# Kernel optimization log

Measured on AMD Instinct MI355X. Metric: run time of the kernel, lower is better.

The kernel has to match this reference:

```python
import jax, jax.numpy as jnp
import numpy as np

MARGIN = 0.3
EPS = 1e-12


def setup_inputs() -> dict:
    key = jax.random.key(0)
    k1, k2, k3, k4 = jax.random.split(key, 4)
    B, N, D = 4, 6400, 32
    pred_masks = jax.random.normal(k1, (B, N, D), dtype=jnp.float32)
    pos_rand = jax.random.uniform(k2, (B, N), dtype=jnp.float32)
    target_gt_idx = jax.random.randint(k3, (B, N), 0, 20, dtype=jnp.int64)
    fg_mask = jax.random.randint(k4, (B, N), 0, 2) > 0
    return {
        "pred_masks": pred_masks,
        "pos_rand": pos_rand,
        "target_gt_idx": target_gt_idx,
        "fg_mask": fg_mask,
    }


def reference(pred_masks, pos_rand, target_gt_idx, fg_mask):
    B, N, D = pred_masks.shape
    # L2-normalize coefficients (F.normalize, eps=1e-12)
    norm = jnp.sqrt(jnp.sum(pred_masks * pred_masks, axis=-1, keepdims=True))
    coeffs = pred_masks / jnp.maximum(norm, EPS)  # [B,N,D]

    valid_pair = fg_mask[:, :, None] & fg_mask[:, None, :]  # [B,N,N]
    same_inst = target_gt_idx[:, :, None] == target_gt_idx[:, None, :]
    eye = jnp.eye(N, dtype=bool)
    S = valid_pair & same_inst & ~eye          # positives (same instance, not self)
    Dm = valid_pair & ~same_inst               # negatives (different instance)

    # Cosine similarities (vectors are unit norm)
    sims = jnp.einsum('bnd,bmd->bnm', coeffs, coeffs)  # [B,N,N]

    # Hardest negative per anchor: argmax similarity among negatives
    neg_idx = jnp.argmax(jnp.where(Dm, sims, -jnp.inf), axis=-1)  # [B,N]
    neg_vec = jnp.take_along_axis(coeffs, neg_idx[..., None], axis=1)  # [B,N,D]

    # Random positive: pick the k-th positive in anchor order, k = floor(u*num_pos)
    num_pos = jnp.sum(S, axis=-1)  # [B,N]
    pos_choice = jnp.floor(pos_rand * num_pos.astype(pos_rand.dtype)).astype(jnp.int32)
    pos_choice = jnp.clip(pos_choice, 0, jnp.maximum(num_pos - 1, 0).astype(jnp.int32))
    cum = jnp.cumsum(S.astype(jnp.int32), axis=-1)  # rank of each positive
    sel = S & (cum == (pos_choice + 1)[..., None])  # one-hot over chosen positive
    pos_idx = jnp.argmax(sel, axis=-1)  # [B,N]
    pos_vec = jnp.take_along_axis(coeffs, pos_idx[..., None], axis=1)  # [B,N,D]

    pos_d = jnp.sqrt(jnp.sum((coeffs - pos_vec) ** 2, axis=-1) + EPS)
    neg_d = jnp.sqrt(jnp.sum((coeffs - neg_vec) ** 2, axis=-1) + EPS)

    valid = fg_mask & (num_pos >= 1) & jnp.any(Dm, axis=-1)  # anchor forms a triplet
    per_anchor = jnp.maximum(pos_d - neg_d + MARGIN, 0.0)
    n_trip = jnp.sum(valid)
    total = jnp.sum(per_anchor * valid.astype(per_anchor.dtype))
    return jnp.where(n_trip > 0, total / jnp.maximum(n_trip, 1).astype(total.dtype), 0.0)
```

## Files before the change

kernel.cpp:

```cpp
#include <hip/hip_runtime.h>
#include <math.h>

#define B_ 4
#define N_ 6400
#define D_ 32
#define TJ 256
#define NCHJ 25
#define TI 128
#define CHUNK 256
#define NCC 25

typedef __attribute__((ext_vector_type(4))) float f32x4;
typedef __attribute__((ext_vector_type(8))) short bf16x8;

static constexpr float MARGIN_ = 0.3f;

__device__ __forceinline__ unsigned fmap(float f) {
    unsigned u = __float_as_uint(f);
    return (u & 0x80000000u) ? ~u : (u | 0x80000000u);
}
__device__ __forceinline__ float funmap(unsigned u) {
    return (u & 0x80000000u) ? __uint_as_float(u ^ 0x80000000u)
                             : __uint_as_float(~u);
}
#define NEG_INF_MAPPED 0x007FFFFFu

__device__ __forceinline__ unsigned short f2bf(float f) {
    unsigned u = __float_as_uint(f);
    unsigned r = u + 0x7fffu + ((u >> 16) & 1u);
    return (unsigned short)(r >> 16);
}
__device__ __forceinline__ float bf2f(unsigned short h) {
    return __uint_as_float(((unsigned)h) << 16);
}
__device__ __forceinline__ void bf2x(unsigned u, float& e0, float& e1) {
    e0 = __uint_as_float(u << 16);
    e1 = __uint_as_float(u & 0xffff0000u);
}

__global__ __launch_bounds__(256) void k_prep(const float* __restrict__ pred,
                                              const int* __restrict__ gt,
                                              const int* __restrict__ fg,
                                              unsigned short* __restrict__ hi_g,
                                              unsigned short* __restrict__ lo_g,
                                              int* __restrict__ clist,
                                              int* __restrict__ cg,
                                              int* __restrict__ Marr,
                                              unsigned* __restrict__ bestArr) {
    int c = blockIdx.x, b = blockIdx.y;
    int t = threadIdx.x;
    int lane = t & 63, w = t >> 6;
    int idx = c * CHUNK + t;

    bestArr[b * N_ + idx] = NEG_INF_MAPPED;

    bool flag = fg[b * N_ + idx] != 0;
    unsigned long long m = __ballot(flag);
    int lp = __popcll(m & ((1ull << lane) - 1ull));
    __shared__ int wsh[4];
    __shared__ int s_off, s_M;
    if (lane == 0) wsh[w] = __popcll(m);

    if (w == 0) {
        int pre = 0, tot = 0;
        #pragma unroll
        for (int cc = 0; cc < NCC; ++cc) {
            const int4 v = ((const int4*)(fg + (size_t)b * N_ + cc * CHUNK))[lane];
            int cnt = (v.x != 0) + (v.y != 0) + (v.z != 0) + (v.w != 0);
            #pragma unroll
            for (int o = 1; o < 64; o <<= 1) cnt += __shfl_xor(cnt, o);
            pre += (cc < c) ? cnt : 0;
            tot += cnt;
        }
        if (lane == 0) { s_off = pre; s_M = tot; }
    }
    __syncthreads();
    if (c == 0 && t == 0) Marr[b] = s_M;
    if (!flag) return;

    int woff = 0;
    #pragma unroll
    for (int k = 0; k < 4; ++k) if (k < w) woff += wsh[k];
    int rank = s_off + woff + lp;
    clist[b * N_ + rank] = idx;
    cg[b * N_ + rank] = gt[b * N_ + idx];

    const float4* s4 = (const float4*)(pred + ((size_t)b * N_ + idx) * D_);
    float f[32];
    float ssq = 0.0f;
    #pragma unroll
    for (int k = 0; k < 8; ++k) {
        float4 q = s4[k];
        f[k * 4] = q.x; f[k * 4 + 1] = q.y; f[k * 4 + 2] = q.z; f[k * 4 + 3] = q.w;
        ssq += q.x * q.x + q.y * q.y + q.z * q.z + q.w * q.w;
    }
    float inv = 1.0f / fmaxf(sqrtf(ssq), 1e-12f);
    unsigned hw[16], lw[16];
    #pragma unroll
    for (int k = 0; k < 16; ++k) {
        float x0 = f[2 * k] * inv, x1 = f[2 * k + 1] * inv;
        unsigned short h0 = f2bf(x0), h1 = f2bf(x1);
        unsigned short l0 = f2bf(x0 - bf2f(h0)), l1 = f2bf(x1 - bf2f(h1));
        hw[k] = (unsigned)h0 | ((unsigned)h1 << 16);
        lw[k] = (unsigned)l0 | ((unsigned)l1 << 16);
    }
    uint4* dh = (uint4*)(hi_g + ((size_t)b * N_ + rank) * 32);
    uint4* dl = (uint4*)(lo_g + ((size_t)b * N_ + rank) * 32);
    #pragma unroll
    for (int k = 0; k < 4; ++k) {
        dh[k] = make_uint4(hw[4 * k], hw[4 * k + 1], hw[4 * k + 2], hw[4 * k + 3]);
        dl[k] = make_uint4(lw[4 * k], lw[4 * k + 1], lw[4 * k + 2], lw[4 * k + 3]);
    }
}

__global__ __launch_bounds__(256) void k_pass(const unsigned short* __restrict__ hi_g,
                                              const unsigned short* __restrict__ lo_g,
                                              const int* __restrict__ cg,
                                              const int* __restrict__ Marr,
                                              unsigned short* __restrict__ p_cnt,
                                              unsigned* __restrict__ bestArr) {
    int b = blockIdx.z;
    int M = Marr[b];
    int i0 = blockIdx.x * TI;
    int j0 = blockIdx.y * TJ;
    if (i0 >= M || j0 >= M) return;

    __shared__ __align__(16) unsigned short sc_hi[TJ * 40];
    __shared__ __align__(16) unsigned short sc_lo[TJ * 40];
    __shared__ int sg[TJ];
    int t = threadIdx.x;

    {
        int j = j0 + t;
        sg[t] = (j < M) ? cg[b * N_ + j] : -1;
    }
    {
        int seg = t & 3, r0 = t >> 2;
        #pragma unroll
        for (int p = 0; p < 4; ++p) {
            int row = p * 64 + r0;
            int j = j0 + row;
            uint4 vh = make_uint4(0u, 0u, 0u, 0u), vl = make_uint4(0u, 0u, 0u, 0u);
            if (j < M) {
                vh = *(const uint4*)(hi_g + ((size_t)b * N_ + j) * 32 + seg * 8);
                vl = *(const uint4*)(lo_g + ((size_t)b * N_ + j) * 32 + seg * 8);
            }
            *(uint4*)(sc_hi + row * 40 + seg * 8) = vh;
            *(uint4*)(sc_lo + row * 40 + seg * 8) = vl;
        }
    }
    __syncthreads();

    int lane = t & 63, w = t >> 6;
    int r = lane & 15, quad = lane >> 4;
    int ib = i0 + w * 32;

    bf16x8 a_hi[2], a_lo[2];
    int gt_i[2][4];
    #pragma unroll
    for (int it = 0; it < 2; ++it) {
        int i = ib + it * 16 + r;
        bf16x8 zh = {0, 0, 0, 0, 0, 0, 0, 0};
        a_hi[it] = zh; a_lo[it] = zh;
        if (i < M) {
            a_hi[it] = *(const bf16x8*)(hi_g + ((size_t)b * N_ + i) * 32 + quad * 8);
            a_lo[it] = *(const bf16x8*)(lo_g + ((size_t)b * N_ + i) * 32 + quad * 8);
        }
        #pragma unroll
        for (int r4 = 0; r4 < 4; ++r4) {
            int ia = ib + it * 16 + quad * 4 + r4;
            gt_i[it][r4] = (ia < M) ? cg[b * N_ + ia] : -2;
        }
    }

    float best[2][4];
    int cnt[2][4];
    #pragma unroll
    for (int it = 0; it < 2; ++it)
        #pragma unroll
        for (int r4 = 0; r4 < 4; ++r4) { best[it][r4] = -INFINITY; cnt[it][r4] = 0; }

    int jrows = min(TJ, M - j0);
    int ntile = (jrows + 15) >> 4;
    for (int jt = 0; jt < ntile; ++jt) {
        int gtj = sg[jt * 16 + r];
        bf16x8 bh = *(const bf16x8*)(sc_hi + (jt * 16 + r) * 40 + quad * 8);
        bf16x8 bl = *(const bf16x8*)(sc_lo + (jt * 16 + r) * 40 + quad * 8);
        bool jv = (gtj >= 0);
        #pragma unroll
        for (int it = 0; it < 2; ++it) {
            f32x4 acc = {0.f, 0.f, 0.f, 0.f};
            acc = __builtin_amdgcn_mfma_f32_16x16x32_bf16(a_hi[it], bh, acc, 0, 0, 0);
            acc = __builtin_amdgcn_mfma_f32_16x16x32_bf16(a_hi[it], bl, acc, 0, 0, 0);
            acc = __builtin_amdgcn_mfma_f32_16x16x32_bf16(a_lo[it], bh, acc, 0, 0, 0);
            #pragma unroll
            for (int r4 = 0; r4 < 4; ++r4) {
                float s = acc[r4];
                bool same = (gtj == gt_i[it][r4]);
                float sm = (same || !jv) ? -INFINITY : s;
                best[it][r4] = fmaxf(best[it][r4], sm);
                cnt[it][r4] += same ? 1 : 0;
            }
        }
    }

    #pragma unroll
    for (int it = 0; it < 2; ++it) {
        #pragma unroll
        for (int r4 = 0; r4 < 4; ++r4) {
            float bb = best[it][r4];
            int cc = cnt[it][r4];
            #pragma unroll
            for (int mk = 1; mk < 16; mk <<= 1) {
                bb = fmaxf(bb, __shfl_xor(bb, mk));
                cc += __shfl_xor(cc, mk);
            }
            if (r == 0) {
                int ia = ib + it * 16 + quad * 4 + r4;
                if (ia < M) {
                    p_cnt[((size_t)b * N_ + ia) * NCHJ + blockIdx.y] = (unsigned short)cc;
                    if (bb > -INFINITY) atomicMax(&bestArr[b * N_ + ia], fmap(bb));
                }
            }
        }
    }
}

__global__ __launch_bounds__(256) void k_combine(const unsigned short* __restrict__ hi_g,
                                                 const unsigned short* __restrict__ lo_g,
                                                 const int* __restrict__ cg,
                                                 const int* __restrict__ clist,
                                                 const int* __restrict__ Marr,
                                                 const float* __restrict__ pos_rand,
                                                 const unsigned short* __restrict__ p_cnt,
                                                 const unsigned* __restrict__ bestArr,
                                                 float* __restrict__ cArr,
                                                 int* __restrict__ vArr) {
    int b = blockIdx.y;
    int M = Marr[b];
    int t = threadIdx.x;
    int w = t >> 6, lane = t & 63;
    int i = blockIdx.x * 4 + w;

    if (i >= M) return;

    float contrib = 0.0f;
    int vflag = 0;

    int nchj = (M + TJ - 1) / TJ;
    int ich = i / TJ;
    const unsigned short* pc = p_cnt + ((size_t)b * N_ + i) * NCHJ;
    int c_s = 0;
    if (lane < nchj) c_s = (int)pc[lane] - (lane == ich ? 1 : 0);
    int P = c_s;
    #pragma unroll
    for (int off = 1; off < 64; off <<= 1) {
        int n = __shfl_up(P, off);
        if (lane >= off) P += n;
    }
    int num_pos = __shfl(P, 63);
    unsigned bu = bestArr[b * N_ + i];
    if (num_pos >= 1 && bu != NEG_INF_MAPPED) {
        float best = funmap(bu);
        int orig = clist[b * N_ + i];
        float u = pos_rand[b * N_ + orig];
        int pcx = (int)floorf(u * (float)num_pos);
        int hi2 = num_pos - 1;
        pcx = pcx < 0 ? 0 : (pcx > hi2 ? hi2 : pcx);
        int target = pcx + 1;
        unsigned long long selm = __ballot(P >= target);
        int sstar = __ffsll((unsigned long long)selm) - 1;
        int c0 = (sstar > 0) ? __shfl(P, sstar - 1) : 0;
        int need = target - c0;
        int jstart = sstar * TJ;
        int jend = min(jstart + TJ, M);
        int ga = cg[b * N_ + i];
        int posj = -1;
        #pragma unroll
        for (int k = 0; k < 4; ++k) {
            if (posj >= 0) continue;
            int j = jstart + k * 64 + lane;
            bool flag = (j < jend) && (cg[b * N_ + j] == ga) && (j != i);
            unsigned long long mk = __ballot(flag);
            int tot = __popcll(mk);
            if (need <= tot) {
                int pfx = __popcll(mk & ((1ull << lane) - 1ull));
                unsigned long long sel = __ballot(flag && (pfx == need - 1));
                posj = jstart + k * 64 + (__ffsll((unsigned long long)sel) - 1);
            } else {
                need -= tot;
            }
        }
        float part = 0.0f;
        if (lane < 16) {
            unsigned xh = ((const unsigned*)(hi_g + ((size_t)b * N_ + i) * 32))[lane];
            unsigned xl = ((const unsigned*)(lo_g + ((size_t)b * N_ + i) * 32))[lane];
            unsigned yh = ((const unsigned*)(hi_g + ((size_t)b * N_ + posj) * 32))[lane];
            unsigned yl = ((const unsigned*)(lo_g + ((size_t)b * N_ + posj) * 32))[lane];
            float a0, a1, b0, b1, c0f, c1f, d0, d1;
            bf2x(xh, a0, a1); bf2x(xl, b0, b1);
            bf2x(yh, c0f, c1f); bf2x(yl, d0, d1);
            part = fmaf(a0 + b0, c0f + d0, (a1 + b1) * (c1f + d1));
        }
        #pragma unroll
        for (int mk2 = 1; mk2 < 16; mk2 <<= 1) part += __shfl_xor(part, mk2);
        float dot = part;
        float pos_d = sqrtf(fmaxf(2.f - 2.f * dot, 0.f) + 1e-12f);
        float neg_d = sqrtf(fmaxf(2.f - 2.f * best, 0.f) + 1e-12f);
        contrib = fmaxf(pos_d - neg_d + MARGIN_, 0.0f);
        vflag = 1;
    }

    if (lane == 0) {
        cArr[b * N_ + i] = contrib;
        vArr[b * N_ + i] = vflag;
    }
}

__global__ __launch_bounds__(1024) void k_final(const float* __restrict__ cArr,
                                                const int* __restrict__ vArr,
                                                const int* __restrict__ Marr,
                                                float* __restrict__ out) {
    int tid = threadIdx.x;
    float tv = 0.0f;
    int tc = 0;
    #pragma unroll
    for (int b = 0; b < B_; ++b) {
        int M = Marr[b];
        for (int i = tid; i < M; i += 1024) {
            tv += cArr[b * N_ + i];
            tc += vArr[b * N_ + i];
        }
    }
    #pragma unroll
    for (int off = 32; off > 0; off >>= 1) {
        tv += __shfl_down(tv, off);
        tc += __shfl_down(tc, off);
    }
    __shared__ float sv[16];
    __shared__ int scnt[16];
    int lane = tid & 63, w = tid >> 6;
    if (lane == 0) { sv[w] = tv; scnt[w] = tc; }
    __syncthreads();
    if (tid == 0) {
        float T = 0.0f; int C = 0;
        #pragma unroll
        for (int k = 0; k < 16; ++k) { T += sv[k]; C += scnt[k]; }
        out[0] = (C > 0) ? (T / (float)C) : 0.0f;
    }
}

extern "C" void kernel_launch(void* const* d_in, const int* in_sizes, int n_in,
                              void* d_out, int out_size, void* d_ws, size_t ws_size,
                              hipStream_t stream) {
    const float* pred     = (const float*)d_in[0];
    const float* pos_rand = (const float*)d_in[1];
    const int*   gt       = (const int*)d_in[2];
    const int*   fg       = (const int*)d_in[3];
    float* out = (float*)d_out;

    char* ws = (char*)d_ws;
    unsigned short* hi_g    = (unsigned short*)(ws);
    unsigned short* lo_g    = (unsigned short*)(ws + 1638400);
    int*            clist   = (int*)(ws + 3276800);
    int*            cg      = (int*)(ws + 3379200);
    int*            Marr    = (int*)(ws + 3481600);
    unsigned*       bestArr = (unsigned*)(ws + 3482688);
    unsigned short* p_cnt   = (unsigned short*)(ws + 3585088);
    float*          cArr    = (float*)(ws + 4865088);
    int*            vArr    = (int*)(ws + 4967488);

    dim3 gpr(NCC, B_);
    k_prep<<<gpr, 256, 0, stream>>>(pred, gt, fg, hi_g, lo_g, clist, cg, Marr, bestArr);
    dim3 gp((N_ + TI - 1) / TI, (N_ + TJ - 1) / TJ, B_);
    k_pass<<<gp, 256, 0, stream>>>(hi_g, lo_g, cg, Marr, p_cnt, bestArr);
    dim3 gc((N_ + 3) / 4, B_);
    k_combine<<<gc, 256, 0, stream>>>(hi_g, lo_g, cg, clist, Marr, pos_rand, p_cnt, bestArr, cArr, vArr);
    k_final<<<1, 1024, 0, stream>>>(cArr, vArr, Marr, out);
}
```

Baseline: 103.6 us.

## Fuse all four stages into one persistent cooperative kernel with grid syncs

Merges the prep, pairwise-pass, combine and final-reduce kernels into a single cooperative kernel of 512 persistent blocks. Grid-wide barriers separate the stages. Work in the pass and combine stages is enumerated only over the valid tiles and anchors, computed from the per-batch foreground counts, so empty blocks are no longer launched. The per-anchor arrays are replaced with per-block partial sums to remove launch overhead and extra memory traffic, at the cost of grid.sync overhead and a fixed grid that may underuse the GPU during the MFMA pass.

```diff
diff --git a/kernel.cpp b/kernel.cpp
--- a/kernel.cpp
+++ b/kernel.cpp
@@ -1,5 +1,8 @@
 #include <hip/hip_runtime.h>
+#include <hip/hip_cooperative_groups.h>
 #include <math.h>
+
+namespace cgrp = cooperative_groups;
 
 #define B_ 4
 #define N_ 6400
@@ -9,6 +12,7 @@
 #define TI 128
 #define CHUNK 256
 #define NCC 25
+#define GRID_ 512
 
 typedef __attribute__((ext_vector_type(4))) float f32x4;
 typedef __attribute__((ext_vector_type(8))) short bf16x8;
@@ -38,315 +42,326 @@
     e1 = __uint_as_float(u & 0xffff0000u);
 }
 
-__global__ __launch_bounds__(256) void k_prep(const float* __restrict__ pred,
-                                              const int* __restrict__ gt,
-                                              const int* __restrict__ fg,
-                                              unsigned short* __restrict__ hi_g,
-                                              unsigned short* __restrict__ lo_g,
-                                              int* __restrict__ clist,
-                                              int* __restrict__ cg,
-                                              int* __restrict__ Marr,
-                                              unsigned* __restrict__ bestArr) {
-    int c = blockIdx.x, b = blockIdx.y;
+__global__ __launch_bounds__(256, 2) void k_mega(const float* __restrict__ pred,
+                                                 const int* __restrict__ gt,
+                                                 const int* __restrict__ fg,
+                                                 const float* __restrict__ pos_rand,
+                                                 unsigned short* __restrict__ hi_g,
+                                                 unsigned short* __restrict__ lo_g,
+                                                 int* __restrict__ clist,
+                                                 int* __restrict__ cgt,
+                                                 int* __restrict__ Marr,
+                                                 unsigned* __restrict__ bestArr,
+                                                 unsigned short* __restrict__ p_cnt,
+                                                 float* __restrict__ partV,
+                                                 int* __restrict__ partC,
+                                                 float* __restrict__ out) {
+    cgrp::grid_group grid = cgrp::this_grid();
     int t = threadIdx.x;
     int lane = t & 63, w = t >> 6;
-    int idx = c * CHUNK + t;
-
-    bestArr[b * N_ + idx] = NEG_INF_MAPPED;
-
-    bool flag = fg[b * N_ + idx] != 0;
-    unsigned long long m = __ballot(flag);
-    int lp = __popcll(m & ((1ull << lane) - 1ull));
-    __shared__ int wsh[4];
-    __shared__ int s_off, s_M;
-    if (lane == 0) wsh[w] = __popcll(m);
-
-    if (w == 0) {
-        int pre = 0, tot = 0;
-        #pragma unroll
-        for (int cc = 0; cc < NCC; ++cc) {
-            const int4 v = ((const int4*)(fg + (size_t)b * N_ + cc * CHUNK))[lane];
-            int cnt = (v.x != 0) + (v.y != 0) + (v.z != 0) + (v.w != 0);
-            #pragma unroll
-            for (int o = 1; o < 64; o <<= 1) cnt += __shfl_xor(cnt, o);
-            pre += (cc < c) ? cnt : 0;
-            tot += cnt;
-        }
-        if (lane == 0) { s_off = pre; s_M = tot; }
-    }
-    __syncthreads();
-    if (c == 0 && t == 0) Marr[b] = s_M;
-    if (!flag) return;
-
-    int woff = 0;
-    #pragma unroll
-    for (int k = 0; k < 4; ++k) if (k < w) woff += wsh[k];
-    int rank = s_off + woff + lp;
-    clist[b * N_ + rank] = idx;
-    cg[b * N_ + rank] = gt[b * N_ + idx];
-
-    const float4* s4 = (const float4*)(pred + ((size_t)b * N_ + idx) * D_);
-    float f[32];
-    float ssq = 0.0f;
-    #pragma unroll
-    for (int k = 0; k < 8; ++k) {
-        float4 q = s4[k];
-        f[k * 4] = q.x; f[k * 4 + 1] = q.y; f[k * 4 + 2] = q.z; f[k * 4 + 3] = q.w;
-        ssq += q.x * q.x + q.y * q.y + q.z * q.z + q.w * q.w;
-    }
-    float inv = 1.0f / fmaxf(sqrtf(ssq), 1e-12f);
-    unsigned hw[16], lw[16];
-    #pragma unroll
-    for (int k = 0; k < 16; ++k) {
-        float x0 = f[2 * k] * inv, x1 = f[2 * k + 1] * inv;
-        unsigned short h0 = f2bf(x0), h1 = f2bf(x1);
-        unsigned short l0 = f2bf(x0 - bf2f(h0)), l1 = f2bf(x1 - bf2f(h1));
-        hw[k] = (unsigned)h0 | ((unsigned)h1 << 16);
-        lw[k] = (unsigned)l0 | ((unsigned)l1 << 16);
-    }
-    uint4* dh = (uint4*)(hi_g + ((size_t)b * N_ + rank) * 32);
-    uint4* dl = (uint4*)(lo_g + ((size_t)b * N_ + rank) * 32);
-    #pragma unroll
-    for (int k = 0; k < 4; ++k) {
-        dh[k] = make_uint4(hw[4 * k], hw[4 * k + 1], hw[4 * k + 2], hw[4 * k + 3]);
-        dl[k] = make_uint4(lw[4 * k], lw[4 * k + 1], lw[4 * k + 2], lw[4 * k + 3]);
-    }
-}
-
-__global__ __launch_bounds__(256) void k_pass(const unsigned short* __restrict__ hi_g,
-                                              const unsigned short* __restrict__ lo_g,
-                                              const int* __restrict__ cg,
-                                              const int* __restrict__ Marr,
-                                              unsigned short* __restrict__ p_cnt,
-                                              unsigned* __restrict__ bestArr) {
-    int b = blockIdx.z;
-    int M = Marr[b];
-    int i0 = blockIdx.x * TI;
-    int j0 = blockIdx.y * TJ;
-    if (i0 >= M || j0 >= M) return;
 
     __shared__ __align__(16) unsigned short sc_hi[TJ * 40];
     __shared__ __align__(16) unsigned short sc_lo[TJ * 40];
     __shared__ int sg[TJ];
-    int t = threadIdx.x;
+    __shared__ int wsh[4];
+    __shared__ int s_off, s_M;
+    __shared__ float swv[4];
+    __shared__ int swc[4];
+
+    for (int u = blockIdx.x; u < NCC * B_; u += gridDim.x) {
+        int c = u % NCC, b = u / NCC;
+        int idx = c * CHUNK + t;
+
+        bestArr[b * N_ + idx] = NEG_INF_MAPPED;
+
+        bool flag = fg[b * N_ + idx] != 0;
+        unsigned long long m = __ballot(flag);
+        int lp = __popcll(m & ((1ull << lane) - 1ull));
+        if (lane == 0) wsh[w] = __popcll(m);
+
+        if (w == 0) {
+            int pre = 0, tot = 0;
+            #pragma unroll
+            for (int cc = 0; cc < NCC; ++cc) {
+                const int4 v = ((const int4*)(fg + (size_t)b * N_ + cc * CHUNK))[lane];
+                int cnt = (v.x != 0) + (v.y != 0) + (v.z != 0) + (v.w != 0);
+                #pragma unroll
+                for (int o = 1; o < 64; o <<= 1) cnt += __shfl_xor(cnt, o);
+                pre += (cc < c) ? cnt : 0;
+                tot += cnt;
+            }
+            if (lane == 0) { s_off = pre; s_M = tot; }
+        }
+        __syncthreads();
+        if (c == 0 && t == 0) Marr[b] = s_M;
+
+        if (flag) {
+            int woff = 0;
+            #pragma unroll
+            for (int k = 0; k < 4; ++k) if (k < w) woff += wsh[k];
+            int rank = s_off + woff + lp;
+            clist[b * N_ + rank] = idx;
+            cgt[b * N_ + rank] = gt[b * N_ + idx];
+
+            const float4* s4 = (const float4*)(pred + ((size_t)b * N_ + idx) * D_);
+            float f[32];
+            float ssq = 0.0f;
+            #pragma unroll
+            for (int k = 0; k < 8; ++k) {
+                float4 q = s4[k];
+                f[k * 4] = q.x; f[k * 4 + 1] = q.y; f[k * 4 + 2] = q.z; f[k * 4 + 3] = q.w;
+                ssq += q.x * q.x + q.y * q.y + q.z * q.z + q.w * q.w;
+            }
+            float inv = 1.0f / fmaxf(sqrtf(ssq), 1e-12f);
+            unsigned hw[16], lw[16];
+            #pragma unroll
+            for (int k = 0; k < 16; ++k) {
+                float x0 = f[2 * k] * inv, x1 = f[2 * k + 1] * inv;
+                unsigned short h0 = f2bf(x0), h1 = f2bf(x1);
+                unsigned short l0 = f2bf(x0 - bf2f(h0)), l1 = f2bf(x1 - bf2f(h1));
+                hw[k] = (unsigned)h0 | ((unsigned)h1 << 16);
+                lw[k] = (unsigned)l0 | ((unsigned)l1 << 16);
+            }
+            uint4* dh = (uint4*)(hi_g + ((size_t)b * N_ + rank) * 32);
+            uint4* dl = (uint4*)(lo_g + ((size_t)b * N_ + rank) * 32);
+            #pragma unroll
+            for (int k = 0; k < 4; ++k) {
+                dh[k] = make_uint4(hw[4 * k], hw[4 * k + 1], hw[4 * k + 2], hw[4 * k + 3]);
+                dl[k] = make_uint4(lw[4 * k], lw[4 * k + 1], lw[4 * k + 2], lw[4 * k + 3]);
+            }
+        }
+        __syncthreads();
+    }
+
+    grid.sync();
+
+    int Mv[B_];
+    #pragma unroll
+    for (int b = 0; b < B_; ++b) Mv[b] = Marr[b];
 
     {
-        int j = j0 + t;
-        sg[t] = (j < M) ? cg[b * N_ + j] : -1;
-    }
-    {
-        int seg = t & 3, r0 = t >> 2;
+        int njv[B_]; int cumU[B_ + 1]; cumU[0] = 0;
         #pragma unroll
-        for (int p = 0; p < 4; ++p) {
-            int row = p * 64 + r0;
-            int j = j0 + row;
-            uint4 vh = make_uint4(0u, 0u, 0u, 0u), vl = make_uint4(0u, 0u, 0u, 0u);
-            if (j < M) {
-                vh = *(const uint4*)(hi_g + ((size_t)b * N_ + j) * 32 + seg * 8);
-                vl = *(const uint4*)(lo_g + ((size_t)b * N_ + j) * 32 + seg * 8);
-            }
-            *(uint4*)(sc_hi + row * 40 + seg * 8) = vh;
-            *(uint4*)(sc_lo + row * 40 + seg * 8) = vl;
-        }
-    }
-    __syncthreads();
-
-    int lane = t & 63, w = t >> 6;
-    int r = lane & 15, quad = lane >> 4;
-    int ib = i0 + w * 32;
-
-    bf16x8 a_hi[2], a_lo[2];
-    int gt_i[2][4];
-    #pragma unroll
-    for (int it = 0; it < 2; ++it) {
-        int i = ib + it * 16 + r;
-        bf16x8 zh = {0, 0, 0, 0, 0, 0, 0, 0};
-        a_hi[it] = zh; a_lo[it] = zh;
-        if (i < M) {
-            a_hi[it] = *(const bf16x8*)(hi_g + ((size_t)b * N_ + i) * 32 + quad * 8);
-            a_lo[it] = *(const bf16x8*)(lo_g + ((size_t)b * N_ + i) * 32 + quad * 8);
-        }
-        #pragma unroll
-        for (int r4 = 0; r4 < 4; ++r4) {
-            int ia = ib + it * 16 + quad * 4 + r4;
-            gt_i[it][r4] = (ia < M) ? cg[b * N_ + ia] : -2;
-        }
-    }
-
-    float best[2][4];
-    int cnt[2][4];
-    #pragma unroll
-    for (int it = 0; it < 2; ++it)
-        #pragma unroll
-        for (int r4 = 0; r4 < 4; ++r4) { best[it][r4] = -INFINITY; cnt[it][r4] = 0; }
-
-    int jrows = min(TJ, M - j0);
-    int ntile = (jrows + 15) >> 4;
-    for (int jt = 0; jt < ntile; ++jt) {
-        int gtj = sg[jt * 16 + r];
-        bf16x8 bh = *(const bf16x8*)(sc_hi + (jt * 16 + r) * 40 + quad * 8);
-        bf16x8 bl = *(const bf16x8*)(sc_lo + (jt * 16 + r) * 40 + quad * 8);
-        bool jv = (gtj >= 0);
-        #pragma unroll
-        for (int it = 0; it < 2; ++it) {
-            f32x4 acc = {0.f, 0.f, 0.f, 0.f};
-            acc = __builtin_amdgcn_mfma_f32_16x16x32_bf16(a_hi[it], bh, acc, 0, 0, 0);
-            acc = __builtin_amdgcn_mfma_f32_16x16x32_bf16(a_hi[it], bl, acc, 0, 0, 0);
-            acc = __builtin_amdgcn_mfma_f32_16x16x32_bf16(a_lo[it], bh, acc, 0, 0, 0);
-            #pragma unroll
-            for (int r4 = 0; r4 < 4; ++r4) {
-                float s = acc[r4];
-                bool same = (gtj == gt_i[it][r4]);
-                float sm = (same || !jv) ? -INFINITY : s;
-                best[it][r4] = fmaxf(best[it][r4], sm);
-                cnt[it][r4] += same ? 1 : 0;
-            }
-        }
-    }
-
-    #pragma unroll
-    for (int it = 0; it < 2; ++it) {
-        #pragma unroll
-        for (int r4 = 0; r4 < 4; ++r4) {
-            float bb = best[it][r4];
-            int cc = cnt[it][r4];
-            #pragma unroll
-            for (int mk = 1; mk < 16; mk <<= 1) {
-                bb = fmaxf(bb, __shfl_xor(bb, mk));
-                cc += __shfl_xor(cc, mk);
-            }
-            if (r == 0) {
-                int ia = ib + it * 16 + quad * 4 + r4;
-                if (ia < M) {
-                    p_cnt[((size_t)b * N_ + ia) * NCHJ + blockIdx.y] = (unsigned short)cc;
-                    if (bb > -INFINITY) atomicMax(&bestArr[b * N_ + ia], fmap(bb));
-                }
-            }
-        }
-    }
-}
-
-__global__ __launch_bounds__(256) void k_combine(const unsigned short* __restrict__ hi_g,
-                                                 const unsigned short* __restrict__ lo_g,
-                                                 const int* __restrict__ cg,
-                                                 const int* __restrict__ clist,
-                                                 const int* __restrict__ Marr,
-                                                 const float* __restrict__ pos_rand,
-                                                 const unsigned short* __restrict__ p_cnt,
-                                                 const unsigned* __restrict__ bestArr,
-                                                 float* __restrict__ cArr,
-                                                 int* __restrict__ vArr) {
-    int b = blockIdx.y;
-    int M = Marr[b];
-    int t = threadIdx.x;
-    int w = t >> 6, lane = t & 63;
-    int i = blockIdx.x * 4 + w;
-
-    if (i >= M) return;
-
-    float contrib = 0.0f;
-    int vflag = 0;
-
-    int nchj = (M + TJ - 1) / TJ;
-    int ich = i / TJ;
-    const unsigned short* pc = p_cnt + ((size_t)b * N_ + i) * NCHJ;
-    int c_s = 0;
-    if (lane < nchj) c_s = (int)pc[lane] - (lane == ich ? 1 : 0);
-    int P = c_s;
-    #pragma unroll
-    for (int off = 1; off < 64; off <<= 1) {
-        int n = __shfl_up(P, off);
-        if (lane >= off) P += n;
-    }
-    int num_pos = __shfl(P, 63);
-    unsigned bu = bestArr[b * N_ + i];
-    if (num_pos >= 1 && bu != NEG_INF_MAPPED) {
-        float best = funmap(bu);
-        int orig = clist[b * N_ + i];
-        float u = pos_rand[b * N_ + orig];
-        int pcx = (int)floorf(u * (float)num_pos);
-        int hi2 = num_pos - 1;
-        pcx = pcx < 0 ? 0 : (pcx > hi2 ? hi2 : pcx);
-        int target = pcx + 1;
-        unsigned long long selm = __ballot(P >= target);
-        int sstar = __ffsll((unsigned long long)selm) - 1;
-        int c0 = (sstar > 0) ? __shfl(P, sstar - 1) : 0;
-        int need = target - c0;
-        int jstart = sstar * TJ;
-        int jend = min(jstart + TJ, M);
-        int ga = cg[b * N_ + i];
-        int posj = -1;
-        #pragma unroll
-        for (int k = 0; k < 4; ++k) {
-            if (posj >= 0) continue;
-            int j = jstart + k * 64 + lane;
-            bool flag = (j < jend) && (cg[b * N_ + j] == ga) && (j != i);
-            unsigned long long mk = __ballot(flag);
-            int tot = __popcll(mk);
-            if (need <= tot) {
-                int pfx = __popcll(mk & ((1ull << lane) - 1ull));
-                unsigned long long sel = __ballot(flag && (pfx == need - 1));
-                posj = jstart + k * 64 + (__ffsll((unsigned long long)sel) - 1);
-            } else {
-                need -= tot;
-            }
-        }
-        float part = 0.0f;
-        if (lane < 16) {
-            unsigned xh = ((const unsigned*)(hi_g + ((size_t)b * N_ + i) * 32))[lane];
-            unsigned xl = ((const unsigned*)(lo_g + ((size_t)b * N_ + i) * 32))[lane];
-            unsigned yh = ((const unsigned*)(hi_g + ((size_t)b * N_ + posj) * 32))[lane];
-            unsigned yl = ((const unsigned*)(lo_g + ((size_t)b * N_ + posj) * 32))[lane];
-            float a0, a1, b0, b1, c0f, c1f, d0, d1;
-            bf2x(xh, a0, a1); bf2x(xl, b0, b1);
-            bf2x(yh, c0f, c1f); bf2x(yl, d0, d1);
-            part = fmaf(a0 + b0, c0f + d0, (a1 + b1) * (c1f + d1));
-        }
-        #pragma unroll
-        for (int mk2 = 1; mk2 < 16; mk2 <<= 1) part += __shfl_xor(part, mk2);
-        float dot = part;
-        float pos_d = sqrtf(fmaxf(2.f - 2.f * dot, 0.f) + 1e-12f);
-        float neg_d = sqrtf(fmaxf(2.f - 2.f * best, 0.f) + 1e-12f);
-        contrib = fmaxf(pos_d - neg_d + MARGIN_, 0.0f);
-        vflag = 1;
-    }
-
-    if (lane == 0) {
-        cArr[b * N_ + i] = contrib;
-        vArr[b * N_ + i] = vflag;
-    }
-}
-
-__global__ __launch_bounds__(1024) void k_final(const float* __restrict__ cArr,
-                                                const int* __restrict__ vArr,
-                                                const int* __restrict__ Marr,
-                                                float* __restrict__ out) {
-    int tid = threadIdx.x;
+        for (int b = 0; b < B_; ++b) {
+            int ni = (Mv[b] + TI - 1) / TI, nj = (Mv[b] + TJ - 1) / TJ;
+            njv[b] = nj; cumU[b + 1] = cumU[b] + ni * nj;
+        }
+        int totU = cumU[B_];
+        for (int u = blockIdx.x; u < totU; u += gridDim.x) {
+            int b = 0;
+            while (u >= cumU[b + 1]) ++b;
+            int ul = u - cumU[b];
+            int ib = ul / njv[b];
+            int jb = ul - ib * njv[b];
+            int M = Mv[b];
+            int i0 = ib * TI, j0 = jb * TJ;
+
+            {
+                int j = j0 + t;
+                sg[t] = (j < M) ? cgt[b * N_ + j] : -1;
+            }
+            {
+                int seg = t & 3, r0 = t >> 2;
+                #pragma unroll
+                for (int p = 0; p < 4; ++p) {
+                    int row = p * 64 + r0;
+                    int j = j0 + row;
+                    uint4 vh = make_uint4(0u, 0u, 0u, 0u), vl = make_uint4(0u, 0u, 0u, 0u);
+                    if (j < M) {
+                        vh = *(const uint4*)(hi_g + ((size_t)b * N_ + j) * 32 + seg * 8);
+                        vl = *(const uint4*)(lo_g + ((size_t)b * N_ + j) * 32 + seg * 8);
+                    }
+                    *(uint4*)(sc_hi + row * 40 + seg * 8) = vh;
+                    *(uint4*)(sc_lo + row * 40 + seg * 8) = vl;
+                }
+            }
+            __syncthreads();
+
+            int r = lane & 15, quad = lane >> 4;
+            int ibase = i0 + w * 32;
+
+            bf16x8 a_hi[2], a_lo[2];
+            int gt_i[2][4];
+            #pragma unroll
+            for (int it = 0; it < 2; ++it) {
+                int i = ibase + it * 16 + r;
+                bf16x8 zh = {0, 0, 0, 0, 0, 0, 0, 0};
+                a_hi[it] = zh; a_lo[it] = zh;
+                if (i < M) {
+                    a_hi[it] = *(const bf16x8*)(hi_g + ((size_t)b * N_ + i) * 32 + quad * 8);
+                    a_lo[it] = *(const bf16x8*)(lo_g + ((size_t)b * N_ + i) * 32 + quad * 8);
+                }
+                #pragma unroll
+                for (int r4 = 0; r4 < 4; ++r4) {
+                    int ia = ibase + it * 16 + quad * 4 + r4;
+                    gt_i[it][r4] = (ia < M) ? cgt[b * N_ + ia] : -2;
+                }
+            }
+
+            float best[2][4];
+            int cnt[2][4];
+            #pragma unroll
+            for (int it = 0; it < 2; ++it)
+                #pragma unroll
+                for (int r4 = 0; r4 < 4; ++r4) { best[it][r4] = -INFINITY; cnt[it][r4] = 0; }
+
+            int jrows = min(TJ, M - j0);
+            int ntile = (jrows + 15) >> 4;
+            for (int jt = 0; jt < ntile; ++jt) {
+                int gtj = sg[jt * 16 + r];
+                bf16x8 bh = *(const bf16x8*)(sc_hi + (jt * 16 + r) * 40 + quad * 8);
+                bf16x8 bl = *(const bf16x8*)(sc_lo + (jt * 16 + r) * 40 + quad * 8);
+                bool jv = (gtj >= 0);
+                #pragma unroll
+                for (int it = 0; it < 2; ++it) {
+                    f32x4 acc = {0.f, 0.f, 0.f, 0.f};
+                    acc = __builtin_amdgcn_mfma_f32_16x16x32_bf16(a_hi[it], bh, acc, 0, 0, 0);
+                    acc = __builtin_amdgcn_mfma_f32_16x16x32_bf16(a_hi[it], bl, acc, 0, 0, 0);
+                    acc = __builtin_amdgcn_mfma_f32_16x16x32_bf16(a_lo[it], bh, acc, 0, 0, 0);
+                    #pragma unroll
+                    for (int r4 = 0; r4 < 4; ++r4) {
+                        float s = acc[r4];
+                        bool same = (gtj == gt_i[it][r4]);
+                        float sm = (same || !jv) ? -INFINITY : s;
+                        best[it][r4] = fmaxf(best[it][r4], sm);
+                        cnt[it][r4] += same ? 1 : 0;
+                    }
+                }
+            }
+
+            #pragma unroll
+            for (int it = 0; it < 2; ++it) {
+                #pragma unroll
+                for (int r4 = 0; r4 < 4; ++r4) {
+                    float bb = best[it][r4];
+                    int cc = cnt[it][r4];
+                    #pragma unroll
+                    for (int mk = 1; mk < 16; mk <<= 1) {
+                        bb = fmaxf(bb, __shfl_xor(bb, mk));
+                        cc += __shfl_xor(cc, mk);
+                    }
+                    if (r == 0) {
+                        int ia = ibase + it * 16 + quad * 4 + r4;
+                        if (ia < M) {
+                            p_cnt[((size_t)b * N_ + ia) * NCHJ + jb] = (unsigned short)cc;
+                            if (bb > -INFINITY) atomicMax(&bestArr[b * N_ + ia], fmap(bb));
+                        }
+                    }
+                }
+            }
+            __syncthreads();
+        }
+    }
+
+    grid.sync();
+
     float tv = 0.0f;
     int tc = 0;
-    #pragma unroll
-    for (int b = 0; b < B_; ++b) {
-        int M = Marr[b];
-        for (int i = tid; i < M; i += 1024) {
-            tv += cArr[b * N_ + i];
-            tc += vArr[b * N_ + i];
-        }
-    }
-    #pragma unroll
-    for (int off = 32; off > 0; off >>= 1) {
-        tv += __shfl_down(tv, off);
-        tc += __shfl_down(tc, off);
-    }
-    __shared__ float sv[16];
-    __shared__ int scnt[16];
-    int lane = tid & 63, w = tid >> 6;
-    if (lane == 0) { sv[w] = tv; scnt[w] = tc; }
+    {
+        int cumC[B_ + 1]; cumC[0] = 0;
+        #pragma unroll
+        for (int b = 0; b < B_; ++b) cumC[b + 1] = cumC[b] + (Mv[b] + 3) / 4;
+        int totC = cumC[B_];
+        for (int u = blockIdx.x; u < totC; u += gridDim.x) {
+            int b = 0;
+            while (u >= cumC[b + 1]) ++b;
+            int g = u - cumC[b];
+            int M = Mv[b];
+            int i = g * 4 + w;
+            if (i < M) {
+                int nchj = (M + TJ - 1) / TJ;
+                int ich = i / TJ;
+                const unsigned short* pc = p_cnt + ((size_t)b * N_ + i) * NCHJ;
+                int c_s = 0;
+                if (lane < nchj) c_s = (int)pc[lane] - (lane == ich ? 1 : 0);
+                int P = c_s;
+                #pragma unroll
+                for (int off = 1; off < 64; off <<= 1) {
+                    int n = __shfl_up(P, off);
+                    if (lane >= off) P += n;
+                }
+                int num_pos = __shfl(P, 63);
+                unsigned bu = bestArr[b * N_ + i];
+                if (num_pos >= 1 && bu != NEG_INF_MAPPED) {
+                    float best = funmap(bu);
+                    int orig = clist[b * N_ + i];
+                    float uu = pos_rand[b * N_ + orig];
+                    int pcx = (int)floorf(uu * (float)num_pos);
+                    int hi2 = num_pos - 1;
+                    pcx = pcx < 0 ? 0 : (pcx > hi2 ? hi2 : pcx);
+                    int target = pcx + 1;
+                    unsigned long long selm = __ballot(P >= target);
+                    int sstar = __ffsll((unsigned long long)selm) - 1;
+                    int c0 = (sstar > 0) ? __shfl(P, sstar - 1) : 0;
+                    int need = target - c0;
+                    int jstart = sstar * TJ;
+                    int jend = min(jstart + TJ, M);
+                    int ga = cgt[b * N_ + i];
+                    int posj = -1;
+                    #pragma unroll
+                    for (int k = 0; k < 4; ++k) {
+                        if (posj >= 0) continue;
+                        int j = jstart + k * 64 + lane;
+                        bool flg = (j < jend) && (cgt[b * N_ + j] == ga) && (j != i);
+                        unsigned long long mk = __ballot(flg);
+                        int tot = __popcll(mk);
+                        if (need <= tot) {
+                            int pfx = __popcll(mk & ((1ull << lane) - 1ull));
+                            unsigned long long sel = __ballot(flg && (pfx == need - 1));
+                            posj = jstart + k * 64 + (__ffsll((unsigned long long)sel) - 1);
+                        } else {
+                            need -= tot;
+                        }
+                    }
+                    float part = 0.0f;
+                    if (lane < 16) {
+                        unsigned xh = ((const unsigned*)(hi_g + ((size_t)b * N_ + i) * 32))[lane];
+                        unsigned xl = ((const unsigned*)(lo_g + ((size_t)b * N_ + i) * 32))[lane];
+                        unsigned yh = ((const unsigned*)(hi_g + ((size_t)b * N_ + posj) * 32))[lane];
+                        unsigned yl = ((const unsigned*)(lo_g + ((size_t)b * N_ + posj) * 32))[lane];
+                        float a0, a1, b0, b1, c0f, c1f, d0, d1;
+                        bf2x(xh, a0, a1); bf2x(xl, b0, b1);
+                        bf2x(yh, c0f, c1f); bf2x(yl, d0, d1);
+                        part = fmaf(a0 + b0, c0f + d0, (a1 + b1) * (c1f + d1));
+                    }
+                    #pragma unroll
+                    for (int mk2 = 1; mk2 < 16; mk2 <<= 1) part += __shfl_xor(part, mk2);
+                    float dot = part;
+                    float pos_d = sqrtf(fmaxf(2.f - 2.f * dot, 0.f) + 1e-12f);
+                    float neg_d = sqrtf(fmaxf(2.f - 2.f * best, 0.f) + 1e-12f);
+                    if (lane == 0) {
+                        tv += fmaxf(pos_d - neg_d + MARGIN_, 0.0f);
+                        tc += 1;
+                    }
+                }
+            }
+        }
+    }
     __syncthreads();
-    if (tid == 0) {
-        float T = 0.0f; int C = 0;
+    if (lane == 0) { swv[w] = tv; swc[w] = tc; }
+    __syncthreads();
+    if (t == 0) {
+        partV[blockIdx.x] = swv[0] + swv[1] + swv[2] + swv[3];
+        partC[blockIdx.x] = swc[0] + swc[1] + swc[2] + swc[3];
+    }
+
+    grid.sync();
+
+    if (blockIdx.x == 0) {
+        float v = 0.0f; int c2 = 0;
+        for (int k = t; k < (int)gridDim.x; k += 256) { v += partV[k]; c2 += partC[k]; }
         #pragma unroll
-        for (int k = 0; k < 16; ++k) { T += sv[k]; C += scnt[k]; }
-        out[0] = (C > 0) ? (T / (float)C) : 0.0f;
+        for (int o = 32; o > 0; o >>= 1) {
+            v += __shfl_down(v, o);
+            c2 += __shfl_down(c2, o);
+        }
+        if (lane == 0) { swv[w] = v; swc[w] = c2; }
+        __syncthreads();
+        if (t == 0) {
+            float T = swv[0] + swv[1] + swv[2] + swv[3];
+            int C = swc[0] + swc[1] + swc[2] + swc[3];
+            out[0] = (C > 0) ? (T / (float)C) : 0.0f;
+        }
     }
 }
 
@@ -357,24 +372,25 @@
     const float* pos_rand = (const float*)d_in[1];
     const int*   gt       = (const int*)d_in[2];
     const int*   fg       = (const int*)d_in[3];
-    float* out = (float*)d_out;
+    float* outp = (float*)d_out;
 
     char* ws = (char*)d_ws;
     unsigned short* hi_g    = (unsigned short*)(ws);
     unsigned short* lo_g    = (unsigned short*)(ws + 1638400);
     int*            clist   = (int*)(ws + 3276800);
-    int*            cg      = (int*)(ws + 3379200);
+    int*            cgt     = (int*)(ws + 3379200);
     int*            Marr    = (int*)(ws + 3481600);
     unsigned*       bestArr = (unsigned*)(ws + 3482688);
     unsigned short* p_cnt   = (unsigned short*)(ws + 3585088);
-    float*          cArr    = (float*)(ws + 4865088);
-    int*            vArr    = (int*)(ws + 4967488);
-
-    dim3 gpr(NCC, B_);
-    k_prep<<<gpr, 256, 0, stream>>>(pred, gt, fg, hi_g, lo_g, clist, cg, Marr, bestArr);
-    dim3 gp((N_ + TI - 1) / TI, (N_ + TJ - 1) / TJ, B_);
-    k_pass<<<gp, 256, 0, stream>>>(hi_g, lo_g, cg, Marr, p_cnt, bestArr);
-    dim3 gc((N_ + 3) / 4, B_);
-    k_combine<<<gc, 256, 0, stream>>>(hi_g, lo_g, cg, clist, Marr, pos_rand, p_cnt, bestArr, cArr, vArr);
-    k_final<<<1, 1024, 0, stream>>>(cArr, vArr, Marr, out);
-}
+    float*          partV   = (float*)(ws + 4865088);
+    int*            partC   = (int*)(ws + 4867136);
+
+    void* kargs[] = {
+        (void*)&pred, (void*)&gt, (void*)&fg, (void*)&pos_rand,
+        (void*)&hi_g, (void*)&lo_g, (void*)&clist, (void*)&cgt,
+        (void*)&Marr, (void*)&bestArr, (void*)&p_cnt,
+        (void*)&partV, (void*)&partC, (void*)&outp
+    };
+    hipLaunchCooperativeKernel((const void*)k_mega, dim3(GRID_), dim3(256),
+                               kargs, 0, stream);
+}
```

After: 265.6 us. +156.4%, slower.

## Fuse final reduction into persistent combine kernel with last-block atomic finish

Applied to the files above, without the earlier changes.

Turns the combine kernel into a grid-stride persistent kernel of 400 blocks. Each block reduces its per-anchor contributions locally, and the last block to finish, detected with an atomic counter, computes the final mean. This removes the separate single-block final kernel and the per-anchor cArr/vArr round trip. Separately, the prep kernel now spreads the foreground chunk counts across all four waves through shared memory instead of making one wave loop over 25 chunks. The cost is atomic counter traffic, a counter reset placed in the prep kernel, and less grid parallelism in the combine stage.

```diff
diff --git a/kernel.cpp b/kernel.cpp
--- a/kernel.cpp
+++ b/kernel.cpp
@@ -9,6 +9,7 @@
 #define TI 128
 #define CHUNK 256
 #define NCC 25
+#define CGRID 400
 
 typedef __attribute__((ext_vector_type(4))) float f32x4;
 typedef __attribute__((ext_vector_type(8))) short bf16x8;
@@ -46,42 +47,48 @@
                                               int* __restrict__ clist,
                                               int* __restrict__ cg,
                                               int* __restrict__ Marr,
-                                              unsigned* __restrict__ bestArr) {
+                                              unsigned* __restrict__ bestArr,
+                                              unsigned* __restrict__ done) {
     int c = blockIdx.x, b = blockIdx.y;
     int t = threadIdx.x;
     int lane = t & 63, w = t >> 6;
     int idx = c * CHUNK + t;
 
+    if (c == 0 && b == 0 && t == 0)
+        __hip_atomic_store(done, 0u, __ATOMIC_RELAXED, __HIP_MEMORY_SCOPE_AGENT);
+
     bestArr[b * N_ + idx] = NEG_INF_MAPPED;
 
     bool flag = fg[b * N_ + idx] != 0;
     unsigned long long m = __ballot(flag);
     int lp = __popcll(m & ((1ull << lane) - 1ull));
     __shared__ int wsh[4];
-    __shared__ int s_off, s_M;
+    __shared__ int scnt[NCC];
     if (lane == 0) wsh[w] = __popcll(m);
 
-    if (w == 0) {
-        int pre = 0, tot = 0;
-        #pragma unroll
-        for (int cc = 0; cc < NCC; ++cc) {
-            const int4 v = ((const int4*)(fg + (size_t)b * N_ + cc * CHUNK))[lane];
-            int cnt = (v.x != 0) + (v.y != 0) + (v.z != 0) + (v.w != 0);
-            #pragma unroll
-            for (int o = 1; o < 64; o <<= 1) cnt += __shfl_xor(cnt, o);
-            pre += (cc < c) ? cnt : 0;
-            tot += cnt;
-        }
-        if (lane == 0) { s_off = pre; s_M = tot; }
+    for (int cc = w; cc < NCC; cc += 4) {
+        const int4 v = ((const int4*)(fg + (size_t)b * N_ + cc * CHUNK))[lane];
+        int cnt = (v.x != 0) + (v.y != 0) + (v.z != 0) + (v.w != 0);
+        #pragma unroll
+        for (int o = 1; o < 64; o <<= 1) cnt += __shfl_xor(cnt, o);
+        if (lane == 0) scnt[cc] = cnt;
     }
     __syncthreads();
-    if (c == 0 && t == 0) Marr[b] = s_M;
+
+    int pre = 0, tot = 0;
+    #pragma unroll
+    for (int cc = 0; cc < NCC; ++cc) {
+        int s = scnt[cc];
+        pre += (cc < c) ? s : 0;
+        tot += s;
+    }
+    if (c == 0 && t == 0) Marr[b] = tot;
     if (!flag) return;
 
     int woff = 0;
     #pragma unroll
     for (int k = 0; k < 4; ++k) if (k < w) woff += wsh[k];
-    int rank = s_off + woff + lp;
+    int rank = pre + woff + lp;
     clist[b * N_ + rank] = idx;
     cg[b * N_ + rank] = gt[b * N_ + idx];
 
@@ -234,119 +241,132 @@
                                                  const float* __restrict__ pos_rand,
                                                  const unsigned short* __restrict__ p_cnt,
                                                  const unsigned* __restrict__ bestArr,
-                                                 float* __restrict__ cArr,
-                                                 int* __restrict__ vArr) {
-    int b = blockIdx.y;
-    int M = Marr[b];
+                                                 float* __restrict__ partV,
+                                                 int* __restrict__ partC,
+                                                 unsigned* __restrict__ done,
+                                                 float* __restrict__ out) {
     int t = threadIdx.x;
     int w = t >> 6, lane = t & 63;
-    int i = blockIdx.x * 4 + w;
-
-    if (i >= M) return;
-
-    float contrib = 0.0f;
-    int vflag = 0;
-
-    int nchj = (M + TJ - 1) / TJ;
-    int ich = i / TJ;
-    const unsigned short* pc = p_cnt + ((size_t)b * N_ + i) * NCHJ;
-    int c_s = 0;
-    if (lane < nchj) c_s = (int)pc[lane] - (lane == ich ? 1 : 0);
-    int P = c_s;
-    #pragma unroll
-    for (int off = 1; off < 64; off <<= 1) {
-        int n = __shfl_up(P, off);
-        if (lane >= off) P += n;
-    }
-    int num_pos = __shfl(P, 63);
-    unsigned bu = bestArr[b * N_ + i];
-    if (num_pos >= 1 && bu != NEG_INF_MAPPED) {
-        float best = funmap(bu);
-        int orig = clist[b * N_ + i];
-        float u = pos_rand[b * N_ + orig];
-        int pcx = (int)floorf(u * (float)num_pos);
-        int hi2 = num_pos - 1;
-        pcx = pcx < 0 ? 0 : (pcx > hi2 ? hi2 : pcx);
-        int target = pcx + 1;
-        unsigned long long selm = __ballot(P >= target);
-        int sstar = __ffsll((unsigned long long)selm) - 1;
-        int c0 = (sstar > 0) ? __shfl(P, sstar - 1) : 0;
-        int need = target - c0;
-        int jstart = sstar * TJ;
-        int jend = min(jstart + TJ, M);
-        int ga = cg[b * N_ + i];
-        int posj = -1;
-        #pragma unroll
-        for (int k = 0; k < 4; ++k) {
-            if (posj >= 0) continue;
-            int j = jstart + k * 64 + lane;
-            bool flag = (j < jend) && (cg[b * N_ + j] == ga) && (j != i);
-            unsigned long long mk = __ballot(flag);
-            int tot = __popcll(mk);
-            if (need <= tot) {
-                int pfx = __popcll(mk & ((1ull << lane) - 1ull));
-                unsigned long long sel = __ballot(flag && (pfx == need - 1));
-                posj = jstart + k * 64 + (__ffsll((unsigned long long)sel) - 1);
-            } else {
-                need -= tot;
-            }
-        }
-        float part = 0.0f;
-        if (lane < 16) {
-            unsigned xh = ((const unsigned*)(hi_g + ((size_t)b * N_ + i) * 32))[lane];
-            unsigned xl = ((const unsigned*)(lo_g + ((size_t)b * N_ + i) * 32))[lane];
-            unsigned yh = ((const unsigned*)(hi_g + ((size_t)b * N_ + posj) * 32))[lane];
-            unsigned yl = ((const unsigned*)(lo_g + ((size_t)b * N_ + posj) * 32))[lane];
-            float a0, a1, b0, b1, c0f, c1f, d0, d1;
-            bf2x(xh, a0, a1); bf2x(xl, b0, b1);
-            bf2x(yh, c0f, c1f); bf2x(yl, d0, d1);
-            part = fmaf(a0 + b0, c0f + d0, (a1 + b1) * (c1f + d1));
-        }
-        #pragma unroll
-        for (int mk2 = 1; mk2 < 16; mk2 <<= 1) part += __shfl_xor(part, mk2);
-        float dot = part;
-        float pos_d = sqrtf(fmaxf(2.f - 2.f * dot, 0.f) + 1e-12f);
-        float neg_d = sqrtf(fmaxf(2.f - 2.f * best, 0.f) + 1e-12f);
-        contrib = fmaxf(pos_d - neg_d + MARGIN_, 0.0f);
-        vflag = 1;
-    }
-
-    if (lane == 0) {
-        cArr[b * N_ + i] = contrib;
-        vArr[b * N_ + i] = vflag;
-    }
-}
-
-__global__ __launch_bounds__(1024) void k_final(const float* __restrict__ cArr,
-                                                const int* __restrict__ vArr,
-                                                const int* __restrict__ Marr,
-                                                float* __restrict__ out) {
-    int tid = threadIdx.x;
+
+    int Mv[B_];
+    int cum[B_ + 1]; cum[0] = 0;
+    #pragma unroll
+    for (int b = 0; b < B_; ++b) {
+        Mv[b] = Marr[b];
+        cum[b + 1] = cum[b] + (Mv[b] + 3) / 4;
+    }
+    int totC = cum[B_];
+
     float tv = 0.0f;
     int tc = 0;
-    #pragma unroll
-    for (int b = 0; b < B_; ++b) {
-        int M = Marr[b];
-        for (int i = tid; i < M; i += 1024) {
-            tv += cArr[b * N_ + i];
-            tc += vArr[b * N_ + i];
-        }
-    }
-    #pragma unroll
-    for (int off = 32; off > 0; off >>= 1) {
-        tv += __shfl_down(tv, off);
-        tc += __shfl_down(tc, off);
-    }
-    __shared__ float sv[16];
-    __shared__ int scnt[16];
-    int lane = tid & 63, w = tid >> 6;
-    if (lane == 0) { sv[w] = tv; scnt[w] = tc; }
+    for (int u = blockIdx.x; u < totC; u += CGRID) {
+        int b = 0;
+        while (u >= cum[b + 1]) ++b;
+        int g = u - cum[b];
+        int M = Mv[b];
+        int i = g * 4 + w;
+        if (i < M) {
+            int nchj = (M + TJ - 1) / TJ;
+            int ich = i / TJ;
+            const unsigned short* pc = p_cnt + ((size_t)b * N_ + i) * NCHJ;
+            int c_s = 0;
+            if (lane < nchj) c_s = (int)pc[lane] - (lane == ich ? 1 : 0);
+            int P = c_s;
+            #pragma unroll
+            for (int off = 1; off < 64; off <<= 1) {
+                int n = __shfl_up(P, off);
+                if (lane >= off) P += n;
+            }
+            int num_pos = __shfl(P, 63);
+            unsigned bu = bestArr[b * N_ + i];
+            if (num_pos >= 1 && bu != NEG_INF_MAPPED) {
+                float best = funmap(bu);
+                int orig = clist[b * N_ + i];
+                float uu = pos_rand[b * N_ + orig];
+                int pcx = (int)floorf(uu * (float)num_pos);
+                int hi2 = num_pos - 1;
+                pcx = pcx < 0 ? 0 : (pcx > hi2 ? hi2 : pcx);
+                int target = pcx + 1;
+                unsigned long long selm = __ballot(P >= target);
+                int sstar = __ffsll((unsigned long long)selm) - 1;
+                int c0 = (sstar > 0) ? __shfl(P, sstar - 1) : 0;
+                int need = target - c0;
+                int jstart = sstar * TJ;
+                int jend = min(jstart + TJ, M);
+                int ga = cg[b * N_ + i];
+                int posj = -1;
+                #pragma unroll
+                for (int k = 0; k < 4; ++k) {
+                    if (posj >= 0) continue;
+                    int j = jstart + k * 64 + lane;
+                    bool flg = (j < jend) && (cg[b * N_ + j] == ga) && (j != i);
+                    unsigned long long mk = __ballot(flg);
+                    int tot = __popcll(mk);
+                    if (need <= tot) {
+                        int pfx = __popcll(mk & ((1ull << lane) - 1ull));
+                        unsigned long long sel = __ballot(flg && (pfx == need - 1));
+                        posj = jstart + k * 64 + (__ffsll((unsigned long long)sel) - 1);
+                    } else {
+                        need -= tot;
+                    }
+                }
+                float part = 0.0f;
+                if (lane < 16) {
+                    unsigned xh = ((const unsigned*)(hi_g + ((size_t)b * N_ + i) * 32))[lane];
+                    unsigned xl = ((const unsigned*)(lo_g + ((size_t)b * N_ + i) * 32))[lane];
+                    unsigned yh = ((const unsigned*)(hi_g + ((size_t)b * N_ + posj) * 32))[lane];
+                    unsigned yl = ((const unsigned*)(lo_g + ((size_t)b * N_ + posj) * 32))[lane];
+                    float a0, a1, b0, b1, c0f, c1f, d0, d1;
+                    bf2x(xh, a0, a1); bf2x(xl, b0, b1);
+                    bf2x(yh, c0f, c1f); bf2x(yl, d0, d1);
+                    part = fmaf(a0 + b0, c0f + d0, (a1 + b1) * (c1f + d1));
+                }
+                #pragma unroll
+                for (int mk2 = 1; mk2 < 16; mk2 <<= 1) part += __shfl_xor(part, mk2);
+                float dot = part;
+                float pos_d = sqrtf(fmaxf(2.f - 2.f * dot, 0.f) + 1e-12f);
+                float neg_d = sqrtf(fmaxf(2.f - 2.f * best, 0.f) + 1e-12f);
+                if (lane == 0) {
+                    tv += fmaxf(pos_d - neg_d + MARGIN_, 0.0f);
+                    tc += 1;
+                }
+            }
+        }
+    }
+
+    __shared__ float swv[4];
+    __shared__ int swc[4];
+    __shared__ int sLast;
+    if (lane == 0) { swv[w] = tv; swc[w] = tc; }
     __syncthreads();
-    if (tid == 0) {
-        float T = 0.0f; int C = 0;
-        #pragma unroll
-        for (int k = 0; k < 16; ++k) { T += sv[k]; C += scnt[k]; }
-        out[0] = (C > 0) ? (T / (float)C) : 0.0f;
+    if (t == 0) {
+        float bv = swv[0] + swv[1] + swv[2] + swv[3];
+        int bc = swc[0] + swc[1] + swc[2] + swc[3];
+        __hip_atomic_store(&partV[blockIdx.x], bv, __ATOMIC_RELAXED, __HIP_MEMORY_SCOPE_AGENT);
+        __hip_atomic_store(&partC[blockIdx.x], bc, __ATOMIC_RELAXED, __HIP_MEMORY_SCOPE_AGENT);
+        unsigned old = __hip_atomic_fetch_add(done, 1u, __ATOMIC_ACQ_REL, __HIP_MEMORY_SCOPE_AGENT);
+        sLast = (old == CGRID - 1) ? 1 : 0;
+    }
+    __syncthreads();
+
+    if (sLast) {
+        float v = 0.0f; int c2 = 0;
+        for (int k = t; k < CGRID; k += 256) {
+            v += __hip_atomic_load(&partV[k], __ATOMIC_RELAXED, __HIP_MEMORY_SCOPE_AGENT);
+            c2 += __hip_atomic_load(&partC[k], __ATOMIC_RELAXED, __HIP_MEMORY_SCOPE_AGENT);
+        }
+        #pragma unroll
+        for (int o = 32; o > 0; o >>= 1) {
+            v += __shfl_down(v, o);
+            c2 += __shfl_down(c2, o);
+        }
+        if (lane == 0) { swv[w] = v; swc[w] = c2; }
+        __syncthreads();
+        if (t == 0) {
+            float T = swv[0] + swv[1] + swv[2] + swv[3];
+            int C = swc[0] + swc[1] + swc[2] + swc[3];
+            out[0] = (C > 0) ? (T / (float)C) : 0.0f;
+        }
     }
 }
 
@@ -367,14 +387,14 @@
     int*            Marr    = (int*)(ws + 3481600);
     unsigned*       bestArr = (unsigned*)(ws + 3482688);
     unsigned short* p_cnt   = (unsigned short*)(ws + 3585088);
-    float*          cArr    = (float*)(ws + 4865088);
-    int*            vArr    = (int*)(ws + 4967488);
+    float*          partV   = (float*)(ws + 4865088);
+    int*            partC   = (int*)(ws + 4866688);
+    unsigned*       done    = (unsigned*)(ws + 4868288);
 
     dim3 gpr(NCC, B_);
-    k_prep<<<gpr, 256, 0, stream>>>(pred, gt, fg, hi_g, lo_g, clist, cg, Marr, bestArr);
+    k_prep<<<gpr, 256, 0, stream>>>(pred, gt, fg, hi_g, lo_g, clist, cg, Marr, bestArr, done);
     dim3 gp((N_ + TI - 1) / TI, (N_ + TJ - 1) / TJ, B_);
     k_pass<<<gp, 256, 0, stream>>>(hi_g, lo_g, cg, Marr, p_cnt, bestArr);
-    dim3 gc((N_ + 3) / 4, B_);
-    k_combine<<<gc, 256, 0, stream>>>(hi_g, lo_g, cg, clist, Marr, pos_rand, p_cnt, bestArr, cArr, vArr);
-    k_final<<<1, 1024, 0, stream>>>(cArr, vArr, Marr, out);
-}
+    k_combine<<<CGRID, 256, 0, stream>>>(hi_g, lo_g, cg, clist, Marr, pos_rand,
+                                         p_cnt, bestArr, partV, partC, done, out);
+}
```

After: 120.1 us. +16.0%, slower.
